# Kernel tuning notes

Hardware: AMD Instinct MI355X
Metric: run time of the kernel (lower is better)

The kernel has to match this reference:

```python
import jax, jax.numpy as jnp
import numpy as np

STRIDE = 1
PAD = 1
K = 3  # kernel size


def setup_inputs() -> dict:
    key = jax.random.key(0)
    k1, k2, k3, k4 = jax.random.split(key, 4)
    B, C, H, W, O = 4, 256, 64, 64, 256
    x = jax.random.normal(k1, (B, C, H, W), jnp.float32)
    offset = jax.random.normal(k2, (B, 2 * K * K, H, W), jnp.float32)
    mask = jax.random.uniform(k3, (B, K * K, H, W), jnp.float32)
    # kaiming-ish scale for the conv weight
    weight = jax.random.normal(k4, (O, C, K, K), jnp.float32) / np.float32(np.sqrt(C * K * K))
    return {"x": x, "offset": offset, "mask": mask, "weight": weight}


def _deform_conv2d(x, offset, mask, weight, stride=STRIDE, pad=PAD):
    """Modulated deformable conv v2 (torchvision deform_conv2d semantics)."""
    B, C, H, W = x.shape
    O, _, Kh, Kw = weight.shape
    KK = Kh * Kw
    Ho = (H + 2 * pad - Kh) // stride + 1
    Wo = (W + 2 * pad - Kw) // stride + 1

    # offset layout: [B, 2*KK, Ho, Wo], pairs are (dy, dx) per kernel tap
    off = offset.reshape(B, KK, 2, Ho, Wo)
    dy, dx = off[:, :, 0], off[:, :, 1]  # [B, KK, Ho, Wo]

    ki = (jnp.arange(KK) // Kw).astype(x.dtype)  # kernel row per tap
    kj = (jnp.arange(KK) % Kw).astype(x.dtype)   # kernel col per tap
    base_y = (jnp.arange(Ho) * stride - pad).astype(x.dtype)
    base_x = (jnp.arange(Wo) * stride - pad).astype(x.dtype)

    # sampling positions [B, KK, Ho, Wo]
    py = base_y[None, None, :, None] + ki[None, :, None, None] + dy
    px = base_x[None, None, None, :] + kj[None, :, None, None] + dx

    y0 = jnp.floor(py)
    x0 = jnp.floor(px)
    wy = py - y0  # fractional weights
    wx = px - x0
    y0i = y0.astype(jnp.int32)
    x0i = x0.astype(jnp.int32)

    x_bhwc = jnp.transpose(x, (0, 2, 3, 1))  # [B, H, W, C] for gathers
    b_idx = jnp.arange(B)[:, None, None, None]

    def gather(yi, xi):
        # zero outside the image (zero-padding bilinear sampling)
        valid = (yi >= 0) & (yi < H) & (xi >= 0) & (xi < W)
        v = x_bhwc[b_idx, jnp.clip(yi, 0, H - 1), jnp.clip(xi, 0, W - 1)]  # [B,KK,Ho,Wo,C]
        return v * valid[..., None].astype(x.dtype)

    one = jnp.asarray(1, x.dtype)
    sampled = (gather(y0i, x0i) * ((one - wy) * (one - wx))[..., None]
               + gather(y0i, x0i + 1) * ((one - wy) * wx)[..., None]
               + gather(y0i + 1, x0i) * (wy * (one - wx))[..., None]
               + gather(y0i + 1, x0i + 1) * (wy * wx)[..., None])

    sampled = sampled * mask.reshape(B, KK, Ho, Wo)[..., None]  # modulation

    # weighted accumulation == implicit GEMM over (c, kk)
    return jnp.einsum('bkhwc,ock->bohw', sampled, weight.reshape(O, C, KK))


def reference(x, offset, mask, weight):
    return _deform_conv2d(x, offset, mask, weight)
```

## Files before the change

### kernel.cpp

```cpp
#include <hip/hip_runtime.h>
#include <hip/hip_bf16.h>

#define CN 256
#define HN 64
#define WN 64
#define ON 256
#define KKN 9
#define HWN 4096
#define KDIM 2304
#define KC 288

using frag_ab = __attribute__((ext_vector_type(8))) short;
using frag_cd = __attribute__((ext_vector_type(4))) float;
using short4v = __attribute__((ext_vector_type(4))) short;
using int4v   = __attribute__((ext_vector_type(4))) int;
using float4v = __attribute__((ext_vector_type(4))) float;
using float2v = __attribute__((ext_vector_type(2))) float;
using uint2v  = __attribute__((ext_vector_type(2))) unsigned;

static __device__ inline short f2bf(float f) {
    union { float f; unsigned u; } v; v.f = f;
    unsigned r = v.u + 0x7fffu + ((v.u >> 16) & 1u);
    return (short)(r >> 16);
}

__global__ __launch_bounds__(256) void prep_kernel(const float* __restrict__ x,
                                                   const float* __restrict__ wsrc,
                                                   short* __restrict__ xb16,
                                                   short* __restrict__ wtb) {
    int bidx = blockIdx.x;
    int tid  = threadIdx.x;
    __shared__ union {
        short tile[128][65];
        short wlds[16][2312];
    } sm;
    if (bidx < 512) {
        int b  = bidx >> 7;
        int rem = bidx & 127;
        int c0 = (rem >> 6) * 128;
        int p0 = (rem & 63) * 64;
        int pl = tid & 63, wq = tid >> 6;
        #pragma unroll
        for (int i = 0; i < 32; ++i) {
            int cl = wq + i * 4;
            sm.tile[cl][pl] =
                f2bf(x[(size_t)(b * CN + c0 + cl) * HWN + p0 + pl]);
        }
        __syncthreads();
        int c4 = (tid & 31) * 4;
        int pb = tid >> 5;
        #pragma unroll
        for (int s = 0; s < 8; ++s) {
            int p = pb + s * 8;
            short4v v;
            v[0] = sm.tile[c4 + 0][p];
            v[1] = sm.tile[c4 + 1][p];
            v[2] = sm.tile[c4 + 2][p];
            v[3] = sm.tile[c4 + 3][p];
            *(short4v*)&xb16[(size_t)(b * HWN + p0 + p) * CN + c0 + c4] = v;
        }
    } else {
        int o0 = (bidx - 512) * 16;
        for (int oi = 0; oi < 16; ++oi) {
            const float* src = &wsrc[(size_t)(o0 + oi) * KDIM + tid * 9];
            short* drow = &sm.wlds[oi][0];
            #pragma unroll
            for (int j = 0; j < 9; ++j)
                drow[j * 256 + tid] = f2bf(src[j]);
        }
        __syncthreads();
        int ob = o0 >> 6, roff = o0 & 63;
        int rl = tid & 15, kc0 = tid >> 4;
        #pragma unroll
        for (int pass = 0; pass < 18; ++pass) {
            int kc  = pass * 16 + kc0;
            int kk  = kc >> 5, oct = kc & 31;
            frag_ab v = *(const frag_ab*)&sm.wlds[rl][kk * 256 + oct * 8];
            *(frag_ab*)&wtb[(size_t)(ob * (KC * 64) + kc * 64 + roff + rl) * 8] = v;
        }
    }
}

__global__ __launch_bounds__(1024, 4) void fused_kernel(const short* __restrict__ xb16,
                                                        const short* __restrict__ wtb,
                                                        const float* __restrict__ offs,
                                                        const float* __restrict__ maskp,
                                                        float* __restrict__ out) {
    __shared__ struct {
        union {
            short Ab[2][16640];
            float outb[64 * 257];
        } mix;
        int desc[4608];
    } sm;
    int tid  = threadIdx.x;
    int bid  = blockIdx.x;
    int wgid = (bid & 7) * 32 + (bid >> 3);
    int m0   = wgid * 64;
    int b    = m0 >> 12;
    int h    = (m0 >> 6) & 63;
    int wv   = __builtin_amdgcn_readfirstlane(tid >> 6);
    int lane = tid & 63;
    int q    = lane >> 4, r = lane & 15;
    int wbase = 65 * (lane >> 1) * 8 + (lane & 1) * 4;
    int lane4 = lane * 4;

    if (tid < 576) {
        int kk = tid >> 6;
        int m  = tid & 63;
        int p  = h * 64 + m;
        int ki = kk / 3, kj = kk - ki * 3;
        float dy = offs[(b * 18 + 2 * kk) * HWN + p];
        float dx = offs[(b * 18 + 2 * kk + 1) * HWN + p];
        float mv = maskp[(b * 9 + kk) * HWN + p];
        float py = (float)(h - 1 + ki) + dy;
        float px = (float)(m - 1 + kj) + dx;
        float y0f = floorf(py), x0f = floorf(px);
        float wy = py - y0f, wx = px - x0f;
        int y0 = (int)y0f, x0 = (int)x0f;
        int4v cb; float4v cw;
        #pragma unroll
        for (int cy = 0; cy < 2; ++cy)
            #pragma unroll
            for (int cx = 0; cx < 2; ++cx) {
                int yy = y0 + cy, xx = x0 + cx;
                bool valid = (yy >= 0 && yy < HN && xx >= 0 && xx < WN);
                int yc = min(max(yy, 0), HN - 1);
                int xc = min(max(xx, 0), WN - 1);
                cb[cy * 2 + cx] = ((b * HN + yc) * WN + xc) * CN;
                float wgt = (cy ? wy : 1.f - wy) * (cx ? wx : 1.f - wx) * mv;
                cw[cy * 2 + cx] = valid ? wgt : 0.f;
            }
        int* dd = &sm.desc[tid * 8];
        *(int4v*)dd       = cb;
        *(float4v*)(dd + 4) = cw;
    }
    __syncthreads();

    bool isP = (wv >= 8);
    int  pw8 = (wv - 8) * 8;

    auto g2 = [&](short4v (&stg)[2][4], int t, int roff) {
        #pragma unroll
        for (int i = 0; i < 2; ++i) {
            int dbase = (t * 64 + pw8 + roff + i) * 8;
            int4v cb = *(const int4v*)&sm.desc[dbase];
            #pragma unroll
            for (int c = 0; c < 4; ++c)
                stg[i][c] = *(const short4v*)&xb16[cb[c] + lane4];
        }
    };
    auto c2 = [&](short4v (&stg)[2][4], short* dstp, int t, int roff) {
        #pragma unroll
        for (int i = 0; i < 2; ++i) {
            int mloc = pw8 + roff + i;
            float4v cw = *(const float4v*)&sm.desc[(t * 64 + mloc) * 8 + 4];
            short4v res;
            #pragma unroll
            for (int g = 0; g < 2; ++g) {
                float2v a = (float2v){0.f, 0.f};
                #pragma unroll
                for (int c = 0; c < 4; ++c) {
                    uint2v uv = __builtin_bit_cast(uint2v, stg[i][c]);
                    unsigned uu = uv[g];
                    float2v f;
                    f.x = __builtin_bit_cast(float, uu << 16);
                    f.y = __builtin_bit_cast(float, uu & 0xffff0000u);
                    a += f * cw[c];
                }
                __hip_bfloat162 p2 = __float22bfloat162_rn(make_float2(a.x, a.y));
                res[2 * g]     = *(short*)&p2.x;
                res[2 * g + 1] = *(short*)&p2.y;
            }
            *(short4v*)&dstp[wbase + mloc * 8] = res;
        }
    };
    auto produce = [&](int t) {
        short* dstp = sm.mix.Ab[t & 1];
        short4v sA[2][4], sB[2][4];
        g2(sA, t, 0);
        g2(sB, t, 2);
        c2(sA, dstp, t, 0);
        g2(sA, t, 4);
        c2(sB, dstp, t, 2);
        g2(sB, t, 6);
        c2(sA, dstp, t, 4);
        c2(sB, dstp, t, 6);
    };

    frag_cd acc[4][2];
    #pragma unroll
    for (int i = 0; i < 4; ++i)
        #pragma unroll
        for (int j = 0; j < 2; ++j)
            acc[i][j] = (frag_cd){0.f, 0.f, 0.f, 0.f};
    int ob = wv >> 1;
    int oh = (wv & 1) * 32;
    auto ld_bf = [&](int kk, int ks, int j) {
        return *(const frag_ab*)
            &wtb[(((size_t)ob * KC + kk * 32 + ks * 4 + q) * 64
                  + oh + j * 16 + r) * 8];
    };
    frag_ab bfx[2][2];
    auto consume = [&](int kk) {
        const short* dstc = sm.mix.Ab[kk & 1];
        #pragma unroll
        for (int ks = 0; ks < 8; ++ks) {
            const int cur = ks & 1;
            frag_ab af[4];
            #pragma unroll
            for (int i = 0; i < 4; ++i)
                af[i] = *(const frag_ab*)
                    &dstc[(65 * (ks * 4 + q) + i * 16 + r) * 8];
            __builtin_amdgcn_s_setprio(1);
            #pragma unroll
            for (int i = 0; i < 4; ++i)
                #pragma unroll
                for (int j = 0; j < 2; ++j)
                    acc[i][j] = __builtin_amdgcn_mfma_f32_16x16x32_bf16(
                        af[i], bfx[cur][j], acc[i][j], 0, 0, 0);
            __builtin_amdgcn_s_setprio(0);
            if (ks < 6) {
                #pragma unroll
                for (int j = 0; j < 2; ++j)
                    bfx[cur][j] = ld_bf(kk, ks + 2, j);
            }
        }
        if (kk < 8) {
            #pragma unroll
            for (int j = 0; j < 2; ++j) {
                bfx[0][j] = ld_bf(kk + 1, 0, j);
                bfx[1][j] = ld_bf(kk + 1, 1, j);
            }
        }
    };

    if (isP) {
        produce(0);
    } else {
        #pragma unroll
        for (int j = 0; j < 2; ++j) {
            bfx[0][j] = ld_bf(0, 0, j);
            bfx[1][j] = ld_bf(0, 1, j);
        }
    }
    asm volatile("s_waitcnt lgkmcnt(0)" ::: "memory");
    __builtin_amdgcn_s_barrier();
    asm volatile("" ::: "memory");

    for (int kk = 0; kk < KKN; ++kk) {
        if (isP) {
            if (kk < 8) produce(kk + 1);
        } else {
            consume(kk);
        }
        asm volatile("s_waitcnt lgkmcnt(0)" ::: "memory");
        __builtin_amdgcn_s_barrier();
        asm volatile("" ::: "memory");
    }

    if (!isP) {
        #pragma unroll
        for (int i = 0; i < 4; ++i)
            #pragma unroll
            for (int j = 0; j < 2; ++j) {
                int ml = i * 16 + q * 4;
                int ol = wv * 32 + j * 16 + r;
                sm.mix.outb[(ml + 0) * 257 + ol] = acc[i][j][0];
                sm.mix.outb[(ml + 1) * 257 + ol] = acc[i][j][1];
                sm.mix.outb[(ml + 2) * 257 + ol] = acc[i][j][2];
                sm.mix.outb[(ml + 3) * 257 + ol] = acc[i][j][3];
            }
    }
    __syncthreads();
    {
        int ww = tid & 63;
        int og = tid >> 6;
        #pragma unroll
        for (int oo = 0; oo < 16; ++oo) {
            int o = oo * 16 + og;
            out[(((size_t)b * ON + o) * HN + h) * WN + ww] =
                sm.mix.outb[ww * 257 + o];
        }
    }
}

extern "C" void kernel_launch(void* const* d_in, const int* in_sizes, int n_in,
                              void* d_out, int out_size, void* d_ws, size_t ws_size,
                              hipStream_t stream) {
    const float* x      = (const float*)d_in[0];
    const float* offset = (const float*)d_in[1];
    const float* mask   = (const float*)d_in[2];
    const float* weight = (const float*)d_in[3];
    float* out = (float*)d_out;

    short* xb16 = (short*)d_ws;
    short* wtb  = (short*)((char*)d_ws + 8388608);

    hipLaunchKernelGGL(prep_kernel,  dim3(528),  dim3(256),  0, stream,
                       x, weight, xb16, wtb);
    hipLaunchKernelGGL(fused_kernel, dim3(256),  dim3(1024), 0, stream,
                       xb16, wtb, offset, mask, out);
}
```

Measured before the change: 118.2 us.

## Split fused deform conv into separate sampling and GEMM kernels

Replaces the single fused kernel, which had producer waves doing bilinear sampling and consumer waves doing MFMA, with two kernels. The first writes the full bf16 im2col matrix (about 75 MB) to workspace with an XOR-swizzled layout. The second streams it into LDS with global_load_lds double buffering and runs a plain GEMM across all 16 waves. This gets rid of the intra-block producer/consumer imbalance, but adds a large round trip through global memory plus an extra launch. The old fused path is kept as a fallback when the workspace is too small.

```diff
diff --git a/kernel.cpp b/kernel.cpp
--- a/kernel.cpp
+++ b/kernel.cpp
@@ -77,6 +77,195 @@
             int kk  = kc >> 5, oct = kc & 31;
             frag_ab v = *(const frag_ab*)&sm.wlds[rl][kk * 256 + oct * 8];
             *(frag_ab*)&wtb[(size_t)(ob * (KC * 64) + kc * 64 + roff + rl) * 8] = v;
+        }
+    }
+}
+
+__global__ __launch_bounds__(256) void sample_kernel(const short* __restrict__ xb16,
+                                                     const float* __restrict__ offs,
+                                                     const float* __restrict__ maskp,
+                                                     short* __restrict__ Ag) {
+    __shared__ int desc[64 * 8];
+    int t   = blockIdx.x;
+    int kk  = blockIdx.y;
+    int tid = threadIdx.x;
+    int b = t >> 6, h = t & 63;
+    if (tid < 64) {
+        int m = tid;
+        int p = h * 64 + m;
+        int ki = kk / 3, kj = kk - ki * 3;
+        float dy = offs[(b * 18 + 2 * kk) * HWN + p];
+        float dx = offs[(b * 18 + 2 * kk + 1) * HWN + p];
+        float mv = maskp[(b * 9 + kk) * HWN + p];
+        float py = (float)(h - 1 + ki) + dy;
+        float px = (float)(m - 1 + kj) + dx;
+        float y0f = floorf(py), x0f = floorf(px);
+        float wy = py - y0f, wx = px - x0f;
+        int y0 = (int)y0f, x0 = (int)x0f;
+        int4v cb; float4v cw;
+        #pragma unroll
+        for (int cy = 0; cy < 2; ++cy)
+            #pragma unroll
+            for (int cx = 0; cx < 2; ++cx) {
+                int yy = y0 + cy, xx = x0 + cx;
+                bool valid = (yy >= 0 && yy < HN && xx >= 0 && xx < WN);
+                int yc = min(max(yy, 0), HN - 1);
+                int xc = min(max(xx, 0), WN - 1);
+                cb[cy * 2 + cx] = ((b * HN + yc) * WN + xc) * CN;
+                float wgt = (cy ? wy : 1.f - wy) * (cx ? wx : 1.f - wx) * mv;
+                cw[cy * 2 + cx] = valid ? wgt : 0.f;
+            }
+        int* dd = &desc[tid * 8];
+        *(int4v*)dd       = cb;
+        *(float4v*)(dd + 4) = cw;
+    }
+    __syncthreads();
+    int wv = tid >> 6, lane = tid & 63;
+    size_t abase = ((size_t)(t * 9 + kk)) << 15;
+    int soff = lane * 8;
+    #pragma unroll
+    for (int i = 0; i < 16; ++i) {
+        int row = wv * 16 + i;
+        int4v   cb = *(const int4v*)&desc[row * 8];
+        float4v cw = *(const float4v*)&desc[row * 8 + 4];
+        short4v stg[4];
+        #pragma unroll
+        for (int c = 0; c < 4; ++c)
+            stg[c] = *(const short4v*)&xb16[cb[c] + lane * 4];
+        short4v res;
+        #pragma unroll
+        for (int g = 0; g < 2; ++g) {
+            float2v a = (float2v){0.f, 0.f};
+            #pragma unroll
+            for (int c = 0; c < 4; ++c) {
+                uint2v uv = __builtin_bit_cast(uint2v, stg[c]);
+                unsigned uu = uv[g];
+                float2v f;
+                f.x = __builtin_bit_cast(float, uu << 16);
+                f.y = __builtin_bit_cast(float, uu & 0xffff0000u);
+                a += f * cw[c];
+            }
+            __hip_bfloat162 p2 = __float22bfloat162_rn(make_float2(a.x, a.y));
+            res[2 * g]     = *(short*)&p2.x;
+            res[2 * g + 1] = *(short*)&p2.y;
+        }
+        int off = (row << 9) + (soff ^ ((row & 7) << 4));
+        *(short4v*)((char*)Ag + abase + off) = res;
+    }
+}
+
+__global__ __launch_bounds__(1024, 1) void gemm_kernel(const short* __restrict__ Ag,
+                                                       const short* __restrict__ wtb,
+                                                       float* __restrict__ out) {
+    __shared__ union {
+        short Ab[2][16384];
+        float outb[64 * 257];
+    } sm;
+    int tid  = threadIdx.x;
+    int bid  = blockIdx.x;
+    int t    = (bid & 7) * 32 + (bid >> 3);
+    int b    = t >> 6, h = t & 63;
+    int wv   = __builtin_amdgcn_readfirstlane(tid >> 6);
+    int lane = tid & 63;
+    int q    = lane >> 4, r = lane & 15;
+    int wg   = wv >> 3;
+    int cg   = wv & 7;
+    int ob   = cg >> 1;
+    int oh   = (cg & 1) * 32;
+    const char* agbase = (const char*)Ag + (((size_t)t * 9) << 15);
+
+    auto stage = [&](int kk, int p) {
+        const char* src = agbase + ((size_t)kk << 15);
+        char* dst = (char*)&sm.Ab[p][0];
+        #pragma unroll
+        for (int rd = 0; rd < 2; ++rd) {
+            int cb = (wv * 64 + rd * 1024) * 16;
+            __builtin_amdgcn_global_load_lds(
+                (const unsigned int*)(src + cb + lane * 16),
+                (unsigned int*)(dst + cb), 16, 0, 0);
+        }
+    };
+
+    frag_cd acc[2][2];
+    #pragma unroll
+    for (int i = 0; i < 2; ++i)
+        #pragma unroll
+        for (int j = 0; j < 2; ++j)
+            acc[i][j] = (frag_cd){0.f, 0.f, 0.f, 0.f};
+
+    auto ld_bf = [&](int kk, int ks, int j) {
+        return *(const frag_ab*)
+            &wtb[(((size_t)ob * KC + kk * 32 + ks * 4 + q) * 64
+                  + oh + j * 16 + r) * 8];
+    };
+    auto consume = [&](int kk, int p) {
+        const char* dstc = (const char*)&sm.Ab[p][0];
+        frag_ab bfx[2][2];
+        #pragma unroll
+        for (int j = 0; j < 2; ++j) {
+            bfx[0][j] = ld_bf(kk, 0, j);
+            bfx[1][j] = ld_bf(kk, 1, j);
+        }
+        #pragma unroll
+        for (int ks = 0; ks < 8; ++ks) {
+            const int cur = ks & 1;
+            frag_ab af[2];
+            #pragma unroll
+            for (int i = 0; i < 2; ++i) {
+                int row = wg * 32 + i * 16 + r;
+                int off = (row << 9)
+                        + ((((ks * 4 + q) << 4)) ^ ((row & 7) << 4));
+                af[i] = *(const frag_ab*)(dstc + off);
+            }
+            __builtin_amdgcn_s_setprio(1);
+            #pragma unroll
+            for (int i = 0; i < 2; ++i)
+                #pragma unroll
+                for (int j = 0; j < 2; ++j)
+                    acc[i][j] = __builtin_amdgcn_mfma_f32_16x16x32_bf16(
+                        af[i], bfx[cur][j], acc[i][j], 0, 0, 0);
+            __builtin_amdgcn_s_setprio(0);
+            if (ks < 6) {
+                #pragma unroll
+                for (int j = 0; j < 2; ++j)
+                    bfx[cur][j] = ld_bf(kk, ks + 2, j);
+            }
+        }
+    };
+
+    stage(0, 0);
+    asm volatile("s_waitcnt vmcnt(0)" ::: "memory");
+    __builtin_amdgcn_s_barrier();
+    asm volatile("" ::: "memory");
+
+    for (int kk = 0; kk < KKN; ++kk) {
+        if (kk < 8) stage(kk + 1, (kk + 1) & 1);
+        consume(kk, kk & 1);
+        asm volatile("s_waitcnt vmcnt(0) lgkmcnt(0)" ::: "memory");
+        __builtin_amdgcn_s_barrier();
+        asm volatile("" ::: "memory");
+    }
+
+    #pragma unroll
+    for (int i = 0; i < 2; ++i)
+        #pragma unroll
+        for (int j = 0; j < 2; ++j) {
+            int ml = wg * 32 + i * 16 + q * 4;
+            int ol = cg * 32 + j * 16 + r;
+            sm.outb[(ml + 0) * 257 + ol] = acc[i][j][0];
+            sm.outb[(ml + 1) * 257 + ol] = acc[i][j][1];
+            sm.outb[(ml + 2) * 257 + ol] = acc[i][j][2];
+            sm.outb[(ml + 3) * 257 + ol] = acc[i][j][3];
+        }
+    __syncthreads();
+    {
+        int ww = tid & 63;
+        int og = tid >> 6;
+        #pragma unroll
+        for (int oo = 0; oo < 16; ++oo) {
+            int o = oo * 16 + og;
+            out[(((size_t)b * ON + o) * HN + h) * WN + ww] =
+                sm.outb[ww * 257 + o];
         }
     }
 }
@@ -140,21 +329,21 @@
     bool isP = (wv >= 8);
     int  pw8 = (wv - 8) * 8;
 
-    auto g2 = [&](short4v (&stg)[2][4], int t, int roff) {
+    auto g2 = [&](short4v (&stg)[2][4], int tt, int roff) {
         #pragma unroll
         for (int i = 0; i < 2; ++i) {
-            int dbase = (t * 64 + pw8 + roff + i) * 8;
+            int dbase = (tt * 64 + pw8 + roff + i) * 8;
             int4v cb = *(const int4v*)&sm.desc[dbase];
             #pragma unroll
             for (int c = 0; c < 4; ++c)
                 stg[i][c] = *(const short4v*)&xb16[cb[c] + lane4];
         }
     };
-    auto c2 = [&](short4v (&stg)[2][4], short* dstp, int t, int roff) {
+    auto c2 = [&](short4v (&stg)[2][4], short* dstp, int tt, int roff) {
         #pragma unroll
         for (int i = 0; i < 2; ++i) {
             int mloc = pw8 + roff + i;
-            float4v cw = *(const float4v*)&sm.desc[(t * 64 + mloc) * 8 + 4];
+            float4v cw = *(const float4v*)&sm.desc[(tt * 64 + mloc) * 8 + 4];
             short4v res;
             #pragma unroll
             for (int g = 0; g < 2; ++g) {
@@ -175,17 +364,17 @@
             *(short4v*)&dstp[wbase + mloc * 8] = res;
         }
     };
-    auto produce = [&](int t) {
-        short* dstp = sm.mix.Ab[t & 1];
+    auto produce = [&](int tt) {
+        short* dstp = sm.mix.Ab[tt & 1];
         short4v sA[2][4], sB[2][4];
-        g2(sA, t, 0);
-        g2(sB, t, 2);
-        c2(sA, dstp, t, 0);
-        g2(sA, t, 4);
-        c2(sB, dstp, t, 2);
-        g2(sB, t, 6);
-        c2(sA, dstp, t, 4);
-        c2(sB, dstp, t, 6);
+        g2(sA, tt, 0);
+        g2(sB, tt, 2);
+        c2(sA, dstp, tt, 0);
+        g2(sA, tt, 4);
+        c2(sB, dstp, tt, 2);
+        g2(sB, tt, 6);
+        c2(sA, dstp, tt, 4);
+        c2(sB, dstp, tt, 6);
     };
 
     frag_cd acc[4][2];
@@ -296,9 +485,17 @@
 
     short* xb16 = (short*)d_ws;
     short* wtb  = (short*)((char*)d_ws + 8388608);
-
-    hipLaunchKernelGGL(prep_kernel,  dim3(528),  dim3(256),  0, stream,
+    short* Ag   = (short*)((char*)d_ws + 16777216);
+
+    hipLaunchKernelGGL(prep_kernel, dim3(528), dim3(256), 0, stream,
                        x, weight, xb16, wtb);
-    hipLaunchKernelGGL(fused_kernel, dim3(256),  dim3(1024), 0, stream,
-                       xb16, wtb, offset, mask, out);
+    if (ws_size >= 92274688u) {
+        hipLaunchKernelGGL(sample_kernel, dim3(256, 9), dim3(256), 0, stream,
+                           xb16, offset, mask, Ag);
+        hipLaunchKernelGGL(gemm_kernel, dim3(256), dim3(1024), 0, stream,
+                           Ag, wtb, out);
+    } else {
+        hipLaunchKernelGGL(fused_kernel, dim3(256), dim3(1024), 0, stream,
+                           xb16, wtb, offset, mask, out);
+    }
 }
```

After: 137.8 us. 16.6% more time.
